# Performance work log

Hardware: AMD Instinct MI355X
Metric: run time of the kernel (lower is better)

Reference implementation:

```python
import jax, jax.numpy as jnp
import numpy as np


def _rel_pos_log(ws):
    coords = np.stack(np.meshgrid(np.arange(ws), np.arange(ws), indexing='ij'))  # [2,ws,ws]
    cf = coords.reshape(2, -1)
    rel = (cf[:, :, None] - cf[:, None, :]).transpose(1, 2, 0).astype(np.float32)  # [N,N,2]
    return np.sign(rel) * np.log1p(np.abs(rel))


def _conv1x1(x, w, b):
    return jnp.einsum('bchw,oc->bohw', x, w) + b[None, :, None, None]


def _conv3x3_reflect(x, w, b):
    xp = jnp.pad(x, ((0, 0), (0, 0), (1, 1), (1, 1)), mode='reflect')
    y = jax.lax.conv_general_dilated(xp, w, (1, 1), 'VALID',
                                     dimension_numbers=('NCHW', 'OIHW', 'NCHW'))
    return y + b[None, :, None, None]


def setup_inputs() -> dict:
    key = jax.random.key(0)
    ks = jax.random.split(key, 8)
    dim, nh = 96, 6
    s = 0.02
    return {
        'X': jax.random.normal(ks[0], (4, dim, 256, 256), jnp.float32),
        'V_w': jax.random.normal(ks[1], (dim, dim), jnp.float32) * s,
        'V_b': jnp.zeros((dim,), jnp.float32),
        'QK_w': jax.random.normal(ks[2], (2 * dim, dim), jnp.float32) * s,
        'QK_b': jnp.zeros((2 * dim,), jnp.float32),
        'meta_w1': jax.random.normal(ks[3], (2, 256), jnp.float32) * 0.1,
        'meta_b1': jnp.zeros((256,), jnp.float32),
        'meta_w2': jax.random.normal(ks[4], (256, nh), jnp.float32) * 0.1,
        'meta_b2': jnp.zeros((nh,), jnp.float32),
        'conv1_w': jax.random.normal(ks[5], (dim, dim, 3, 3), jnp.float32) * s,
        'conv1_b': jnp.zeros((dim,), jnp.float32),
        'conv2_w': jax.random.normal(ks[6], (dim, dim, 3, 3), jnp.float32) * s,
        'conv2_b': jnp.zeros((dim,), jnp.float32),
        'proj_w': jax.random.normal(ks[7], (dim, dim), jnp.float32) * s,
        'proj_b': jnp.zeros((dim,), jnp.float32),
        'window_size': 8,
        'num_heads': 6,
    }


def reference(X, V_w, V_b, QK_w, QK_b, meta_w1, meta_b1, meta_w2, meta_b2,
              conv1_w, conv1_b, conv2_w, conv2_b, proj_w, proj_b,
              window_size, num_heads):
    B, C, H, W = X.shape
    ws = int(window_size)
    nh = int(num_heads)
    hd = C // nh
    scale = hd ** (-0.5)

    V = _conv1x1(X, V_w, V_b)                     # [B,C,H,W]
    QK = _conv1x1(X, QK_w, QK_b)                  # [B,2C,H,W]
    QKV = jnp.concatenate([QK, V], axis=1)        # [B,3C,H,W]

    # window partition (shift_size=0, H,W divisible by ws -> no padding)
    x = QKV.transpose(0, 2, 3, 1)                 # [B,H,W,3C]
    x = x.reshape(B, H // ws, ws, W // ws, ws, 3 * C)
    x = x.transpose(0, 1, 3, 2, 4, 5).reshape(-1, ws * ws, 3 * C)  # [nW,N,3C]

    qkv = x.reshape(-1, ws * ws, 3, nh, hd).transpose(2, 0, 3, 1, 4)
    q, k, v = qkv[0] * scale, qkv[1], qkv[2]      # [nW,nh,N,hd]
    attn = jnp.einsum('bhnd,bhmd->bhnm', q, k)    # [nW,nh,N,N]

    rp = jnp.asarray(_rel_pos_log(ws))            # [N,N,2]
    bias = jax.nn.relu(rp @ meta_w1 + meta_b1) @ meta_w2 + meta_b2  # [N,N,nh]
    attn = attn + bias.transpose(2, 0, 1)[None]
    attn = jax.nn.softmax(attn, axis=-1)

    o = jnp.einsum('bhnm,bhmd->bhnd', attn, v)    # [nW,nh,N,hd]
    o = o.transpose(0, 2, 1, 3).reshape(-1, ws * ws, C)

    # window reverse
    o = o.reshape(B, H // ws, W // ws, ws, ws, C)
    o = o.transpose(0, 1, 3, 2, 4, 5).reshape(B, H, W, C)
    attn_out = o.transpose(0, 3, 1, 2)            # [B,C,H,W]

    conv_out = _conv3x3_reflect(jax.nn.relu(_conv3x3_reflect(V, conv1_w, conv1_b)),
                                conv2_w, conv2_b)
    out = _conv1x1(conv_out + attn_out, proj_w, proj_b)
    return out
```

## Files before the change

### kernel.cpp

```cpp
#include <hip/hip_runtime.h>
#include <cmath>

typedef short  short8 __attribute__((ext_vector_type(8)));
typedef float  f32x4  __attribute__((ext_vector_type(4)));
typedef unsigned short us8 __attribute__((ext_vector_type(8)));
typedef unsigned short us4 __attribute__((ext_vector_type(4)));

constexpr int kHW = 65536;
constexpr int kP  = 262144;

__device__ __forceinline__ unsigned short f2bf(float x) {
  unsigned u = __builtin_bit_cast(unsigned, x);
  u += 0x7fffu + ((u >> 16) & 1u);
  return (unsigned short)(u >> 16);
}
__device__ __forceinline__ float bf2f(unsigned short h) {
  unsigned u = ((unsigned)h) << 16;
  return __builtin_bit_cast(float, u);
}
__device__ __forceinline__ void split2(float v, unsigned short& h, unsigned short& l) {
  unsigned short hh = f2bf(v);
  h = hh;
  l = f2bf(v - bf2f(hh));
}
__device__ __forceinline__ void gload16(const void* g, void* l) {
  __builtin_amdgcn_global_load_lds(
      (const __attribute__((address_space(1))) void*)g,
      (__attribute__((address_space(3))) void*)l, 16, 0, 0);
}

__global__ void bias_kernel(const float* __restrict__ w1, const float* __restrict__ b1,
                            const float* __restrict__ w2, const float* __restrict__ b2,
                            float* __restrict__ bias_tab) {
  int i = blockIdx.x;
  int j = threadIdx.x;
  float dy = (float)((i >> 3) - (j >> 3));
  float dx = (float)((i & 7) - (j & 7));
  float r0 = copysignf(log1pf(fabsf(dy)), dy);
  float r1 = copysignf(log1pf(fabsf(dx)), dx);
  float acc[6];
#pragma unroll
  for (int h = 0; h < 6; ++h) acc[h] = b2[h];
  for (int t = 0; t < 256; ++t) {
    float hv = fmaf(r0, w1[t], fmaf(r1, w1[256 + t], b1[t]));
    hv = fmaxf(hv, 0.f);
#pragma unroll
    for (int h = 0; h < 6; ++h) acc[h] = fmaf(hv, w2[t * 6 + h], acc[h]);
  }
#pragma unroll
  for (int h = 0; h < 6; ++h) bias_tab[h * 4096 + i * 64 + j] = acc[h];
}

__global__ void prep_weights(const float* __restrict__ qk_w, const float* __restrict__ v_w,
                             const float* __restrict__ c1w, const float* __restrict__ c2w,
                             const float* __restrict__ pjw,
                             unsigned short* __restrict__ Wqh, unsigned short* __restrict__ Wql,
                             unsigned short* __restrict__ W1h,
                             unsigned short* __restrict__ W2h,
                             unsigned short* __restrict__ Wph, unsigned short* __restrict__ Wpl) {
  int i = blockIdx.x * 256 + threadIdx.x;
  if (i < 27648) {
    float v = (i < 18432) ? qk_w[i] : v_w[i - 18432];
    split2(v, Wqh[i], Wql[i]);
  }
  if (i < 82944) {
    int dlt = i / 9216;
    int oc  = (i / 96) % 96;
    int ic  = i % 96;
    int src = (oc * 96 + ic) * 9 + dlt;
    W1h[i] = f2bf(c1w[src]);
    W2h[i] = f2bf(c2w[src]);
  }
  if (i < 9216) split2(pjw[i], Wph[i], Wpl[i]);
}

__global__ __launch_bounds__(256) void split_x(const float* __restrict__ X,
                                               unsigned short* __restrict__ Xh) {
  __shared__ float tile[96][65];
  int t = threadIdx.x;
  size_t p0 = (size_t)blockIdx.x * 64;
  int b = (int)(p0 >> 16), pix = (int)(p0 & 65535);
  const float* xb = X + (size_t)b * 96 * kHW + pix;
#pragma unroll
  for (int i = 0; i < 24; ++i) {
    int ic = (t >> 6) + i * 4;
    tile[ic][t & 63] = xb[(size_t)ic * kHW + (t & 63)];
  }
  __syncthreads();
  int px = t >> 2;
  size_t outbase = (p0 + px) * 96;
#pragma unroll
  for (int cc = 0; cc < 3; ++cc) {
    int c = (t & 3) + cc * 4;
    us8 h8;
#pragma unroll
    for (int j = 0; j < 8; ++j) h8[j] = f2bf(tile[c * 8 + j][px]);
    *(us8*)(Xh + outbase + c * 8) = h8;
  }
}

__global__ __launch_bounds__(256, 2) void qkv_gemm(
    const unsigned short* __restrict__ Wqh, const unsigned short* __restrict__ Wql,
    const unsigned short* __restrict__ Xh,
    const float* __restrict__ qk_b, const float* __restrict__ v_b,
    unsigned short* __restrict__ Qp, unsigned short* __restrict__ Kp,
    unsigned short* __restrict__ Vp) {
  int t = threadIdx.x, wv = t >> 6, lane = t & 63;
  size_t px0 = (size_t)blockIdx.x * 256 + wv * 64;
  int col = lane & 15, g = lane >> 4;

  const char* bH = (const char*)Xh + ((px0 + col) * 96 + g * 8) * 2;
  short8 Bh[3][4];
#pragma unroll
  for (int ks = 0; ks < 3; ++ks)
#pragma unroll
    for (int nf = 0; nf < 4; ++nf)
      Bh[ks][nf] = *(const short8*)(bH + (size_t)(nf * 16 * 96 + ks * 32) * 2);

#pragma unroll 1
  for (int z = 0; z < 3; ++z) {
    f32x4 acc[6][4];
#pragma unroll
    for (int m = 0; m < 6; ++m)
#pragma unroll
      for (int n = 0; n < 4; ++n) acc[m][n] = (f32x4)0.f;
    const char* aH = (const char*)(Wqh + z * 9216) + (size_t)(col * 96 + g * 8) * 2;
    const char* aL = (const char*)(Wql + z * 9216) + (size_t)(col * 96 + g * 8) * 2;
#pragma unroll
    for (int ks = 0; ks < 3; ++ks) {
      short8 Ah[6], Al[6];
#pragma unroll
      for (int mf = 0; mf < 6; ++mf) {
        Ah[mf] = *(const short8*)(aH + (size_t)(mf * 16 * 96 + ks * 32) * 2);
        Al[mf] = *(const short8*)(aL + (size_t)(mf * 16 * 96 + ks * 32) * 2);
      }
#pragma unroll
      for (int mf = 0; mf < 6; ++mf)
#pragma unroll
        for (int nf = 0; nf < 4; ++nf) {
          acc[mf][nf] = __builtin_amdgcn_mfma_f32_16x16x32_bf16(Ah[mf], Bh[ks][nf], acc[mf][nf], 0, 0, 0);
          acc[mf][nf] = __builtin_amdgcn_mfma_f32_16x16x32_bf16(Al[mf], Bh[ks][nf], acc[mf][nf], 0, 0, 0);
        }
    }
    const float* bias = (z == 0) ? qk_b : (z == 1 ? qk_b + 96 : v_b);
    float scale = (z == 0) ? 0.25f : 1.f;
    unsigned short* dst = (z == 0) ? Qp : (z == 1 ? Kp : Vp);
#pragma unroll
    for (int mf = 0; mf < 6; ++mf) {
      int oc0 = mf * 16 + g * 4;
      f32x4 bv;
#pragma unroll
      for (int r = 0; r < 4; ++r) bv[r] = bias[oc0 + r];
#pragma unroll
      for (int nf = 0; nf < 4; ++nf) {
        size_t p = px0 + nf * 16 + col;
        f32x4 v = (acc[mf][nf] + bv) * scale;
        us4 o;
#pragma unroll
        for (int r = 0; r < 4; ++r) o[r] = f2bf(v[r]);
        *(us4*)(dst + ((size_t)mf * kP + p) * 16 + g * 4) = o;
      }
    }
  }
}

__global__ __launch_bounds__(256) void attn_mfma(
    const unsigned short* __restrict__ Qp, const unsigned short* __restrict__ Kp,
    const unsigned short* __restrict__ Vp, const float* __restrict__ bias_tab,
    unsigned short* __restrict__ out) {
  __shared__ unsigned short PT[4][64 * 72];
  __shared__ unsigned short VT[4][16 * 72];
  __shared__ float rls[4][64];

  int t = threadIdx.x;
  int wv = t >> 6, lane = t & 63;
  int l15 = lane & 15, g = lane >> 4;
  int h = blockIdx.y;
  int wid = blockIdx.x * 4 + wv;
  int b = wid >> 10, wy = (wid >> 5) & 31, wx = wid & 31;
  size_t p0 = ((size_t)b << 16) + (size_t)wy * 8 * 256 + (size_t)wx * 8;
  const float* bt = bias_tab + h * 4096;

  f32x4 acc[4][4];
#pragma unroll
  for (int kf = 0; kf < 4; ++kf)
#pragma unroll
    for (int qf = 0; qf < 4; ++qf)
      acc[kf][qf] = *(const f32x4*)(bt + (qf * 16 + l15) * 64 + kf * 16 + g * 4);

  short8 Af[4], Bf[4];
#pragma unroll
  for (int f = 0; f < 4; ++f) {
    int kk = f * 16 + l15;
    size_t pk = p0 + (size_t)(kk >> 3) * 256 + (kk & 7);
    if (g < 2) {
      Af[f] = *(const short8*)(Kp + ((size_t)h * kP + pk) * 16 + g * 8);
      Bf[f] = *(const short8*)(Qp + ((size_t)h * kP + pk) * 16 + g * 8);
    } else {
      Af[f] = (short8)0;
      Bf[f] = (short8)0;
    }
  }

  {
    size_t pv = p0 + (size_t)(lane >> 3) * 256 + (lane & 7);
    const unsigned short* vp = Vp + ((size_t)h * kP + pv) * 16;
    us8 v0 = *(const us8*)(vp), v1 = *(const us8*)(vp + 8);
    unsigned short* vt = VT[wv];
#pragma unroll
    for (int d = 0; d < 8; ++d) {
      vt[d * 72 + lane]       = v0[d];
      vt[(d + 8) * 72 + lane] = v1[d];
    }
  }

#pragma unroll
  for (int kf = 0; kf < 4; ++kf)
#pragma unroll
    for (int qf = 0; qf < 4; ++qf)
      acc[kf][qf] = __builtin_amdgcn_mfma_f32_16x16x32_bf16(Af[kf], Bf[qf], acc[kf][qf], 0, 0, 0);

#pragma unroll
  for (int qf = 0; qf < 4; ++qf) {
    float m = acc[0][qf][0];
#pragma unroll
    for (int kf = 0; kf < 4; ++kf)
#pragma unroll
      for (int r = 0; r < 4; ++r) m = fmaxf(m, acc[kf][qf][r]);
    m = fmaxf(m, __shfl_xor(m, 16));
    m = fmaxf(m, __shfl_xor(m, 32));
    float sum = 0.f;
#pragma unroll
    for (int kf = 0; kf < 4; ++kf)
#pragma unroll
      for (int r = 0; r < 4; ++r) {
        float pe = __expf(acc[kf][qf][r] - m);
        acc[kf][qf][r] = pe;
        sum += pe;
      }
    sum += __shfl_xor(sum, 16);
    sum += __shfl_xor(sum, 32);
    if (g == 0) rls[wv][qf * 16 + l15] = 1.f / sum;
  }

  unsigned short* pt = PT[wv];
#pragma unroll
  for (int qf = 0; qf < 4; ++qf)
#pragma unroll
    for (int kf = 0; kf < 4; ++kf) {
      us4 pb;
#pragma unroll
      for (int r = 0; r < 4; ++r) pb[r] = f2bf(acc[kf][qf][r]);
      *(us4*)&pt[(qf * 16 + l15) * 72 + kf * 16 + g * 4] = pb;
    }

  short8 Pa[4][2], Vb[2];
#pragma unroll
  for (int qf = 0; qf < 4; ++qf)
#pragma unroll
    for (int kc = 0; kc < 2; ++kc)
      Pa[qf][kc] = *(const short8*)&pt[(qf * 16 + l15) * 72 + kc * 32 + g * 8];
#pragma unroll
  for (int kc = 0; kc < 2; ++kc)
    Vb[kc] = *(const short8*)&VT[wv][l15 * 72 + kc * 32 + g * 8];
  f32x4 o[4];
#pragma unroll
  for (int qf = 0; qf < 4; ++qf) {
    o[qf] = (f32x4)0.f;
#pragma unroll
    for (int kc = 0; kc < 2; ++kc)
      o[qf] = __builtin_amdgcn_mfma_f32_16x16x32_bf16(Pa[qf][kc], Vb[kc], o[qf], 0, 0, 0);
  }

#pragma unroll
  for (int qf = 0; qf < 4; ++qf) {
    f32x4 rv = *(const f32x4*)&rls[wv][qf * 16 + g * 4];
#pragma unroll
    for (int r = 0; r < 4; ++r)
      pt[(qf * 16 + g * 4 + r) * 72 + l15] = f2bf(o[qf][r] * rv[r]);
  }
  {
    int q = lane;
    us8 o0 = *(const us8*)&pt[q * 72];
    us8 o1 = *(const us8*)&pt[q * 72 + 8];
    size_t pq = p0 + (size_t)(q >> 3) * 256 + (q & 7);
    unsigned short* op = out + ((size_t)h * kP + pq) * 16;
    *(us8*)(op)     = o0;
    *(us8*)(op + 8) = o1;
  }
}

constexpr int kChunks = 1560;
constexpr int kSlotB  = 26624;

__device__ __forceinline__ void stage_rows(const char* __restrict__ rowbase,
                                           char* slot, const int (&off)[7], int t) {
  int wvbase = t & 192;
#pragma unroll
  for (int i = 0; i < 7; ++i) {
    if (i < 6 || t < 24)
      gload16(rowbase + off[i], slot + (i * 256 + wvbase) * 16);
  }
}

__device__ __forceinline__ void conv_dy(
    const char* __restrict__ lds, const unsigned short* __restrict__ Wh,
    int tap0, int och, int xq, int col, int g, f32x4 (&acc)[3][4]) {
#pragma unroll
  for (int dx = 0; dx < 3; ++dx) {
    const char* ah = (const char*)Wh + ((size_t)(tap0 + dx) * 9216 + och * 4608 + col * 96 + g * 8) * 2;
    int ppb = xq * 64 + col + dx;
#pragma unroll
    for (int ks = 0; ks < 3; ++ks) {
      short8 Ah[3], Bf[4];
#pragma unroll
      for (int mf = 0; mf < 3; ++mf)
        Ah[mf] = *(const short8*)(ah + (size_t)(mf * 16 * 96 + ks * 32) * 2);
#pragma unroll
      for (int nf = 0; nf < 4; ++nf) {
        int pp = ppb + nf * 16;
        Bf[nf] = *(const short8*)(lds + ks * 8320 + ((g ^ (pp & 3)) * 2080) + pp * 16);
      }
#pragma unroll
      for (int mf = 0; mf < 3; ++mf)
#pragma unroll
        for (int nf = 0; nf < 4; ++nf)
          acc[mf][nf] = __builtin_amdgcn_mfma_f32_16x16x32_bf16(Ah[mf], Bf[nf], acc[mf][nf], 0, 0, 0);
    }
  }
}

template <int MODE>
__global__ __launch_bounds__(256, 2) void conv_gl(
    const unsigned short* __restrict__ Wh,
    const unsigned short* __restrict__ B_, const float* __restrict__ bias,
    const unsigned short* __restrict__ attn, unsigned short* __restrict__ O_) {
  __shared__ char lds[3][kSlotB];
  int t = threadIdx.x, wv = t >> 6, lane = t & 63;
  int col = lane & 15, g = lane >> 4;
  int och = wv >> 1, xq = wv & 1;
  int bid = blockIdx.x;
  int g8 = (bid & 7) * 256 + (bid >> 3);
  int xh = g8 & 1;
  int ry = g8 >> 1;
  int b = ry >> 8, y = ry & 255;
  int x0 = xh * 128;

  int off[7];
#pragma unroll
  for (int i = 0; i < 7; ++i) {
    int idx = i * 256 + t;
    int ks = idx / 520;
    int rem = idx - ks * 520;
    int gp = rem / 130;
    int pp = rem - gp * 130;
    int c8 = ks * 4 + (gp ^ (pp & 3));
    int xx = x0 - 1 + pp;
    xx = xx < 0 ? 1 : (xx > 255 ? 254 : xx);
    if (MODE == 0)
      off[i] = (((c8 >> 1) * kP + xx) * 16 + (c8 & 1) * 8) * 2;
    else
      off[i] = (xx * 96 + c8 * 8) * 2;
  }

  const size_t rowBytes = (MODE == 0) ? (size_t)256 * 32 : (size_t)256 * 192;
  const char* Bbase = (const char*)B_ + (size_t)b * kHW * ((MODE == 0) ? 32 : 192);
  int ym = (y == 0) ? 1 : y - 1;
  int yp = (y == 255) ? 254 : y + 1;

  stage_rows(Bbase + (size_t)ym * rowBytes, lds[0], off, t);
  stage_rows(Bbase + (size_t)y  * rowBytes, lds[1], off, t);
  stage_rows(Bbase + (size_t)yp * rowBytes, lds[2], off, t);
  __syncthreads();

  f32x4 acc[3][4];
#pragma unroll
  for (int m = 0; m < 3; ++m)
#pragma unroll
    for (int n = 0; n < 4; ++n) acc[m][n] = (f32x4)0.f;

  conv_dy(lds[0], Wh, 0, och, xq, col, g, acc);
  conv_dy(lds[1], Wh, 3, och, xq, col, g, acc);
  conv_dy(lds[2], Wh, 6, och, xq, col, g, acc);
  __syncthreads();

  char* tb = lds[0];
  size_t prow = (size_t)b * kHW + (size_t)y * 256;
#pragma unroll
  for (int mf = 0; mf < 3; ++mf) {
    int oc0 = och * 48 + mf * 16 + g * 4;
    f32x4 bv;
#pragma unroll
    for (int r = 0; r < 4; ++r) bv[r] = bias[oc0 + r];
#pragma unroll
    for (int nf = 0; nf < 4; ++nf) {
      int pp = xq * 64 + nf * 16 + col;
      f32x4 v = acc[mf][nf] + bv;
      if (MODE == 0) {
#pragma unroll
        for (int r = 0; r < 4; ++r) v[r] = fmaxf(v[r], 0.f);
      } else {
        size_t p = prow + x0 + pp;
        us4 a4 = *(const us4*)(attn + ((size_t)(och * 3 + mf) * kP + p) * 16 + g * 4);
#pragma unroll
        for (int r = 0; r < 4; ++r) v[r] += bf2f(a4[r]);
      }
      us4 o;
#pragma unroll
      for (int r = 0; r < 4; ++r) o[r] = f2bf(v[r]);
      *(us4*)(tb + pp * 208 + oc0 * 2) = o;
    }
  }
  __syncthreads();
  {
    int pp = t >> 1, half = t & 1;
    const char* src = tb + pp * 208 + half * 96;
    us8 o0 = *(const us8*)(src);
    us8 o1 = *(const us8*)(src + 16);
    us8 o2 = *(const us8*)(src + 32);
    us8 o3 = *(const us8*)(src + 48);
    us8 o4 = *(const us8*)(src + 64);
    us8 o5 = *(const us8*)(src + 80);
    unsigned short* dst = O_ + (prow + x0) * 96 + (size_t)t * 48;
    *(us8*)(dst)      = o0;
    *(us8*)(dst + 8)  = o1;
    *(us8*)(dst + 16) = o2;
    *(us8*)(dst + 24) = o3;
    *(us8*)(dst + 32) = o4;
    *(us8*)(dst + 40) = o5;
  }
}

__global__ __launch_bounds__(256, 2) void proj_gemm(
    const unsigned short* __restrict__ Wph, const unsigned short* __restrict__ Wpl,
    const unsigned short* __restrict__ S_, const float* __restrict__ bias,
    float* __restrict__ out) {
  int t = threadIdx.x, wv = t >> 6, lane = t & 63;
  size_t px0 = (size_t)blockIdx.x * 256 + wv * 64;
  int col = lane & 15, g = lane >> 4;
  f32x4 acc[6][4];
#pragma unroll
  for (int m = 0; m < 6; ++m)
#pragma unroll
    for (int n = 0; n < 4; ++n) acc[m][n] = (f32x4)0.f;
  const char* aH = (const char*)Wph + (size_t)(col * 96 + g * 8) * 2;
  const char* aL = (const char*)Wpl + (size_t)(col * 96 + g * 8) * 2;
  const char* bH = (const char*)S_ + ((px0 + col) * 96 + g * 8) * 2;
#pragma unroll
  for (int ks = 0; ks < 3; ++ks) {
    short8 Ah[6], Al[6], Bf[4];
#pragma unroll
    for (int mf = 0; mf < 6; ++mf) {
      Ah[mf] = *(const short8*)(aH + (size_t)(mf * 16 * 96 + ks * 32) * 2);
      Al[mf] = *(const short8*)(aL + (size_t)(mf * 16 * 96 + ks * 32) * 2);
    }
#pragma unroll
    for (int nf = 0; nf < 4; ++nf)
      Bf[nf] = *(const short8*)(bH + (size_t)(nf * 16 * 96 + ks * 32) * 2);
#pragma unroll
    for (int mf = 0; mf < 6; ++mf)
#pragma unroll
      for (int nf = 0; nf < 4; ++nf) {
        acc[mf][nf] = __builtin_amdgcn_mfma_f32_16x16x32_bf16(Ah[mf], Bf[nf], acc[mf][nf], 0, 0, 0);
        acc[mf][nf] = __builtin_amdgcn_mfma_f32_16x16x32_bf16(Al[mf], Bf[nf], acc[mf][nf], 0, 0, 0);
      }
  }
#pragma unroll
  for (int mf = 0; mf < 6; ++mf) {
    int oc0 = mf * 16 + g * 4;
#pragma unroll
    for (int nf = 0; nf < 4; ++nf) {
      size_t p = px0 + nf * 16 + col;
      size_t bb = p >> 16, pix = p & 65535;
      f32x4 v = acc[mf][nf];
#pragma unroll
      for (int r = 0; r < 4; ++r)
        out[(bb * 96 + oc0 + r) * (size_t)kHW + pix] = v[r] + bias[oc0 + r];
    }
  }
}

extern "C" void kernel_launch(void* const* d_in, const int* in_sizes, int n_in,
                              void* d_out, int out_size, void* d_ws, size_t ws_size,
                              hipStream_t stream) {
  const float* X       = (const float*)d_in[0];
  const float* V_w     = (const float*)d_in[1];
  const float* V_b     = (const float*)d_in[2];
  const float* QK_w    = (const float*)d_in[3];
  const float* QK_b    = (const float*)d_in[4];
  const float* meta_w1 = (const float*)d_in[5];
  const float* meta_b1 = (const float*)d_in[6];
  const float* meta_w2 = (const float*)d_in[7];
  const float* meta_b2 = (const float*)d_in[8];
  const float* conv1_w = (const float*)d_in[9];
  const float* conv1_b = (const float*)d_in[10];
  const float* conv2_w = (const float*)d_in[11];
  const float* conv2_b = (const float*)d_in[12];
  const float* proj_w  = (const float*)d_in[13];
  const float* proj_b  = (const float*)d_in[14];
  float* out = (float*)d_out;

  char* w = (char*)d_ws;
  const size_t PLANE = (size_t)kP * 96 * 2;
  unsigned short* Xh = (unsigned short*)(w + 0 * PLANE);
  unsigned short* Qp = (unsigned short*)(w + 1 * PLANE);
  unsigned short* Kp = (unsigned short*)(w + 2 * PLANE);
  unsigned short* Vp = (unsigned short*)(w + 3 * PLANE);
  float* bias_tab    = (float*)(w + 4 * PLANE);
  unsigned short* Wqh = (unsigned short*)(w + 4 * PLANE + 98304);
  unsigned short* Wql = Wqh + 27648;
  unsigned short* W1h = Wql + 27648;
  unsigned short* W2h = W1h + 82944;
  unsigned short* Wph = W2h + 82944;
  unsigned short* Wpl = Wph + 9216;
  unsigned short* T1r = Xh;
  unsigned short* S2r = Qp;
  unsigned short* attnB = (unsigned short*)out;

  bias_kernel<<<dim3(64), dim3(64), 0, stream>>>(meta_w1, meta_b1, meta_w2, meta_b2, bias_tab);
  prep_weights<<<dim3(324), dim3(256), 0, stream>>>(QK_w, V_w, conv1_w, conv2_w, proj_w,
                                                    Wqh, Wql, W1h, W2h, Wph, Wpl);
  split_x<<<dim3(4096), dim3(256), 0, stream>>>(X, Xh);
  qkv_gemm<<<dim3(1024), dim3(256), 0, stream>>>(Wqh, Wql, Xh, QK_b, V_b, Qp, Kp, Vp);
  attn_mfma<<<dim3(1024, 6), dim3(256), 0, stream>>>(Qp, Kp, Vp, bias_tab, attnB);
  conv_gl<0><<<dim3(2048), dim3(256), 0, stream>>>(W1h, Vp, conv1_b, nullptr, T1r);
  conv_gl<1><<<dim3(2048), dim3(256), 0, stream>>>(W2h, T1r, conv2_b, attnB, S2r);
  proj_gemm<<<dim3(1024), dim3(256), 0, stream>>>(Wph, Wpl, S2r, proj_b, out);
}
```

Baseline: 366.4 us.

## Switch intermediates to 8-channel planar layout and drop LDS staging in convs

Changes the Q/K/V, attention output, conv intermediates and conv-to-proj buffers from pixel-major (16- or 96-channel interleaved) to planes of 8 channels. This lets each MFMA lane load a 16-byte B fragment straight from global memory. The 3x3 conv kernels drop the global_load_lds row staging, the LDS transpose-for-store and the syncthreads, and read neighbours directly from global/L2 with higher occupancy (launch bounds 4). The trade-off is redundant global loads for the overlapping taps, now served by cache instead of shared memory, and stores that scatter across 12 planes.

```diff
diff --git a/kernel.cpp b/kernel.cpp
--- a/kernel.cpp
+++ b/kernel.cpp
@@ -22,11 +22,6 @@
   unsigned short hh = f2bf(v);
   h = hh;
   l = f2bf(v - bf2f(hh));
-}
-__device__ __forceinline__ void gload16(const void* g, void* l) {
-  __builtin_amdgcn_global_load_lds(
-      (const __attribute__((address_space(1))) void*)g,
-      (__attribute__((address_space(3))) void*)l, 16, 0, 0);
 }
 
 __global__ void bias_kernel(const float* __restrict__ w1, const float* __restrict__ b1,
@@ -148,6 +143,7 @@
 #pragma unroll
     for (int mf = 0; mf < 6; ++mf) {
       int oc0 = mf * 16 + g * 4;
+      int c8 = mf * 2 + (g >> 1);
       f32x4 bv;
 #pragma unroll
       for (int r = 0; r < 4; ++r) bv[r] = bias[oc0 + r];
@@ -158,7 +154,7 @@
         us4 o;
 #pragma unroll
         for (int r = 0; r < 4; ++r) o[r] = f2bf(v[r]);
-        *(us4*)(dst + ((size_t)mf * kP + p) * 16 + g * 4) = o;
+        *(us4*)(dst + ((size_t)c8 * kP + p) * 8 + (g & 1) * 4) = o;
       }
     }
   }
@@ -194,8 +190,9 @@
     int kk = f * 16 + l15;
     size_t pk = p0 + (size_t)(kk >> 3) * 256 + (kk & 7);
     if (g < 2) {
-      Af[f] = *(const short8*)(Kp + ((size_t)h * kP + pk) * 16 + g * 8);
-      Bf[f] = *(const short8*)(Qp + ((size_t)h * kP + pk) * 16 + g * 8);
+      size_t pl = (size_t)(2 * h + g) * kP;
+      Af[f] = *(const short8*)(Kp + (pl + pk) * 8);
+      Bf[f] = *(const short8*)(Qp + (pl + pk) * 8);
     } else {
       Af[f] = (short8)0;
       Bf[f] = (short8)0;
@@ -204,8 +201,8 @@
 
   {
     size_t pv = p0 + (size_t)(lane >> 3) * 256 + (lane & 7);
-    const unsigned short* vp = Vp + ((size_t)h * kP + pv) * 16;
-    us8 v0 = *(const us8*)(vp), v1 = *(const us8*)(vp + 8);
+    us8 v0 = *(const us8*)(Vp + ((size_t)(2 * h) * kP + pv) * 8);
+    us8 v1 = *(const us8*)(Vp + ((size_t)(2 * h + 1) * kP + pv) * 8);
     unsigned short* vt = VT[wv];
 #pragma unroll
     for (int d = 0; d < 8; ++d) {
@@ -284,58 +281,16 @@
     us8 o0 = *(const us8*)&pt[q * 72];
     us8 o1 = *(const us8*)&pt[q * 72 + 8];
     size_t pq = p0 + (size_t)(q >> 3) * 256 + (q & 7);
-    unsigned short* op = out + ((size_t)h * kP + pq) * 16;
-    *(us8*)(op)     = o0;
-    *(us8*)(op + 8) = o1;
-  }
-}
-
-constexpr int kChunks = 1560;
-constexpr int kSlotB  = 26624;
-
-__device__ __forceinline__ void stage_rows(const char* __restrict__ rowbase,
-                                           char* slot, const int (&off)[7], int t) {
-  int wvbase = t & 192;
-#pragma unroll
-  for (int i = 0; i < 7; ++i) {
-    if (i < 6 || t < 24)
-      gload16(rowbase + off[i], slot + (i * 256 + wvbase) * 16);
-  }
-}
-
-__device__ __forceinline__ void conv_dy(
-    const char* __restrict__ lds, const unsigned short* __restrict__ Wh,
-    int tap0, int och, int xq, int col, int g, f32x4 (&acc)[3][4]) {
-#pragma unroll
-  for (int dx = 0; dx < 3; ++dx) {
-    const char* ah = (const char*)Wh + ((size_t)(tap0 + dx) * 9216 + och * 4608 + col * 96 + g * 8) * 2;
-    int ppb = xq * 64 + col + dx;
-#pragma unroll
-    for (int ks = 0; ks < 3; ++ks) {
-      short8 Ah[3], Bf[4];
-#pragma unroll
-      for (int mf = 0; mf < 3; ++mf)
-        Ah[mf] = *(const short8*)(ah + (size_t)(mf * 16 * 96 + ks * 32) * 2);
-#pragma unroll
-      for (int nf = 0; nf < 4; ++nf) {
-        int pp = ppb + nf * 16;
-        Bf[nf] = *(const short8*)(lds + ks * 8320 + ((g ^ (pp & 3)) * 2080) + pp * 16);
-      }
-#pragma unroll
-      for (int mf = 0; mf < 3; ++mf)
-#pragma unroll
-        for (int nf = 0; nf < 4; ++nf)
-          acc[mf][nf] = __builtin_amdgcn_mfma_f32_16x16x32_bf16(Ah[mf], Bf[nf], acc[mf][nf], 0, 0, 0);
-    }
+    *(us8*)(out + ((size_t)(2 * h) * kP + pq) * 8)     = o0;
+    *(us8*)(out + ((size_t)(2 * h + 1) * kP + pq) * 8) = o1;
   }
 }
 
 template <int MODE>
-__global__ __launch_bounds__(256, 2) void conv_gl(
+__global__ __launch_bounds__(256, 4) void conv_direct(
     const unsigned short* __restrict__ Wh,
     const unsigned short* __restrict__ B_, const float* __restrict__ bias,
     const unsigned short* __restrict__ attn, unsigned short* __restrict__ O_) {
-  __shared__ char lds[3][kSlotB];
   int t = threadIdx.x, wv = t >> 6, lane = t & 63;
   int col = lane & 15, g = lane >> 4;
   int och = wv >> 1, xq = wv & 1;
@@ -344,34 +299,16 @@
   int xh = g8 & 1;
   int ry = g8 >> 1;
   int b = ry >> 8, y = ry & 255;
-  int x0 = xh * 128;
-
-  int off[7];
-#pragma unroll
-  for (int i = 0; i < 7; ++i) {
-    int idx = i * 256 + t;
-    int ks = idx / 520;
-    int rem = idx - ks * 520;
-    int gp = rem / 130;
-    int pp = rem - gp * 130;
-    int c8 = ks * 4 + (gp ^ (pp & 3));
-    int xx = x0 - 1 + pp;
-    xx = xx < 0 ? 1 : (xx > 255 ? 254 : xx);
-    if (MODE == 0)
-      off[i] = (((c8 >> 1) * kP + xx) * 16 + (c8 & 1) * 8) * 2;
-    else
-      off[i] = (xx * 96 + c8 * 8) * 2;
-  }
-
-  const size_t rowBytes = (MODE == 0) ? (size_t)256 * 32 : (size_t)256 * 192;
-  const char* Bbase = (const char*)B_ + (size_t)b * kHW * ((MODE == 0) ? 32 : 192);
-  int ym = (y == 0) ? 1 : y - 1;
-  int yp = (y == 255) ? 254 : y + 1;
-
-  stage_rows(Bbase + (size_t)ym * rowBytes, lds[0], off, t);
-  stage_rows(Bbase + (size_t)y  * rowBytes, lds[1], off, t);
-  stage_rows(Bbase + (size_t)yp * rowBytes, lds[2], off, t);
-  __syncthreads();
+  int x0 = xh * 128 + xq * 64;
+
+  int xc[4][3];
+#pragma unroll
+  for (int nf = 0; nf < 4; ++nf)
+#pragma unroll
+    for (int dx = 0; dx < 3; ++dx) {
+      int xx = x0 + nf * 16 + col + dx - 1;
+      xc[nf][dx] = xx < 0 ? 1 : (xx > 255 ? 254 : xx);
+    }
 
   f32x4 acc[3][4];
 #pragma unroll
@@ -379,55 +316,60 @@
 #pragma unroll
     for (int n = 0; n < 4; ++n) acc[m][n] = (f32x4)0.f;
 
-  conv_dy(lds[0], Wh, 0, och, xq, col, g, acc);
-  conv_dy(lds[1], Wh, 3, och, xq, col, g, acc);
-  conv_dy(lds[2], Wh, 6, och, xq, col, g, acc);
-  __syncthreads();
-
-  char* tb = lds[0];
-  size_t prow = (size_t)b * kHW + (size_t)y * 256;
+  size_t bb = (size_t)b * kHW;
+#pragma unroll
+  for (int dy = 0; dy < 3; ++dy) {
+    int yy = y + dy - 1;
+    yy = yy < 0 ? 1 : (yy > 255 ? 254 : yy);
+    size_t rowp = bb + (size_t)yy * 256;
+#pragma unroll
+    for (int dx = 0; dx < 3; ++dx) {
+      const char* ah = (const char*)Wh +
+          ((size_t)(dy * 3 + dx) * 9216 + och * 4608 + col * 96 + g * 8) * 2;
+#pragma unroll
+      for (int ks = 0; ks < 3; ++ks) {
+        short8 Ah[3], Bf[4];
+#pragma unroll
+        for (int mf = 0; mf < 3; ++mf)
+          Ah[mf] = *(const short8*)(ah + (size_t)(mf * 16 * 96 + ks * 32) * 2);
+        size_t plane = (size_t)(ks * 4 + g) * kP;
+#pragma unroll
+        for (int nf = 0; nf < 4; ++nf)
+          Bf[nf] = *(const short8*)(B_ + (plane + rowp + xc[nf][dx]) * 8);
+#pragma unroll
+        for (int mf = 0; mf < 3; ++mf)
+#pragma unroll
+          for (int nf = 0; nf < 4; ++nf)
+            acc[mf][nf] = __builtin_amdgcn_mfma_f32_16x16x32_bf16(Ah[mf], Bf[nf], acc[mf][nf], 0, 0, 0);
+      }
+    }
+  }
+
+  size_t prow = bb + (size_t)y * 256;
 #pragma unroll
   for (int mf = 0; mf < 3; ++mf) {
     int oc0 = och * 48 + mf * 16 + g * 4;
+    int c8o = och * 6 + mf * 2 + (g >> 1);
     f32x4 bv;
 #pragma unroll
     for (int r = 0; r < 4; ++r) bv[r] = bias[oc0 + r];
 #pragma unroll
     for (int nf = 0; nf < 4; ++nf) {
-      int pp = xq * 64 + nf * 16 + col;
+      size_t p = prow + x0 + nf * 16 + col;
       f32x4 v = acc[mf][nf] + bv;
       if (MODE == 0) {
 #pragma unroll
         for (int r = 0; r < 4; ++r) v[r] = fmaxf(v[r], 0.f);
       } else {
-        size_t p = prow + x0 + pp;
-        us4 a4 = *(const us4*)(attn + ((size_t)(och * 3 + mf) * kP + p) * 16 + g * 4);
+        us4 a4 = *(const us4*)(attn + ((size_t)c8o * kP + p) * 8 + (g & 1) * 4);
 #pragma unroll
         for (int r = 0; r < 4; ++r) v[r] += bf2f(a4[r]);
       }
       us4 o;
 #pragma unroll
       for (int r = 0; r < 4; ++r) o[r] = f2bf(v[r]);
-      *(us4*)(tb + pp * 208 + oc0 * 2) = o;
-    }
-  }
-  __syncthreads();
-  {
-    int pp = t >> 1, half = t & 1;
-    const char* src = tb + pp * 208 + half * 96;
-    us8 o0 = *(const us8*)(src);
-    us8 o1 = *(const us8*)(src + 16);
-    us8 o2 = *(const us8*)(src + 32);
-    us8 o3 = *(const us8*)(src + 48);
-    us8 o4 = *(const us8*)(src + 64);
-    us8 o5 = *(const us8*)(src + 80);
-    unsigned short* dst = O_ + (prow + x0) * 96 + (size_t)t * 48;
-    *(us8*)(dst)      = o0;
-    *(us8*)(dst + 8)  = o1;
-    *(us8*)(dst + 16) = o2;
-    *(us8*)(dst + 24) = o3;
-    *(us8*)(dst + 32) = o4;
-    *(us8*)(dst + 40) = o5;
+      *(us4*)(O_ + ((size_t)c8o * kP + p) * 8 + (g & 1) * 4) = o;
+    }
   }
 }
 
@@ -445,7 +387,6 @@
     for (int n = 0; n < 4; ++n) acc[m][n] = (f32x4)0.f;
   const char* aH = (const char*)Wph + (size_t)(col * 96 + g * 8) * 2;
   const char* aL = (const char*)Wpl + (size_t)(col * 96 + g * 8) * 2;
-  const char* bH = (const char*)S_ + ((px0 + col) * 96 + g * 8) * 2;
 #pragma unroll
   for (int ks = 0; ks < 3; ++ks) {
     short8 Ah[6], Al[6], Bf[4];
@@ -454,9 +395,10 @@
       Ah[mf] = *(const short8*)(aH + (size_t)(mf * 16 * 96 + ks * 32) * 2);
       Al[mf] = *(const short8*)(aL + (size_t)(mf * 16 * 96 + ks * 32) * 2);
     }
+    size_t plane = (size_t)(ks * 4 + g) * kP;
 #pragma unroll
     for (int nf = 0; nf < 4; ++nf)
-      Bf[nf] = *(const short8*)(bH + (size_t)(nf * 16 * 96 + ks * 32) * 2);
+      Bf[nf] = *(const short8*)(S_ + (plane + px0 + nf * 16 + col) * 8);
 #pragma unroll
     for (int mf = 0; mf < 6; ++mf)
 #pragma unroll
@@ -513,8 +455,8 @@
   unsigned short* W2h = W1h + 82944;
   unsigned short* Wph = W2h + 82944;
   unsigned short* Wpl = Wph + 9216;
-  unsigned short* T1r = Xh;
-  unsigned short* S2r = Qp;
+  unsigned short* T1c = Xh;
+  unsigned short* S2c = Qp;
   unsigned short* attnB = (unsigned short*)out;
 
   bias_kernel<<<dim3(64), dim3(64), 0, stream>>>(meta_w1, meta_b1, meta_w2, meta_b2, bias_tab);
@@ -523,7 +465,7 @@
   split_x<<<dim3(4096), dim3(256), 0, stream>>>(X, Xh);
   qkv_gemm<<<dim3(1024), dim3(256), 0, stream>>>(Wqh, Wql, Xh, QK_b, V_b, Qp, Kp, Vp);
   attn_mfma<<<dim3(1024, 6), dim3(256), 0, stream>>>(Qp, Kp, Vp, bias_tab, attnB);
-  conv_gl<0><<<dim3(2048), dim3(256), 0, stream>>>(W1h, Vp, conv1_b, nullptr, T1r);
-  conv_gl<1><<<dim3(2048), dim3(256), 0, stream>>>(W2h, T1r, conv2_b, attnB, S2r);
-  proj_gemm<<<dim3(1024), dim3(256), 0, stream>>>(Wph, Wpl, S2r, proj_b, out);
-}
+  conv_direct<0><<<dim3(2048), dim3(256), 0, stream>>>(W1h, Vp, conv1_b, nullptr, T1c);
+  conv_direct<1><<<dim3(2048), dim3(256), 0, stream>>>(W2h, T1c, conv2_b, attnB, S2c);
+  proj_gemm<<<dim3(1024), dim3(256), 0, stream>>>(Wph, Wpl, S2c, proj_b, out);
+}
```

Result: slower. 390.0 us (+6.4%).
